# Performance work log

Hardware: AMD Instinct MI355X
Metric: run time of the kernel (lower is better)

The kernel has to match this reference:

```python
import jax, jax.numpy as jnp
import numpy as np

B, S, D, H = 2, 2048, 1024, 16  # batch, seq, rep_dim, num_heads
DH = D // H
MASK_VALUE = -1e-06  # value passed by MHAttention to masked_softmax (NOT -1e6)


def setup_inputs() -> dict:
    key = jax.random.key(0)
    ks = jax.random.split(key, 16)
    def xavier(k, shape):
        fan_in, fan_out = shape[0], shape[1]
        limit = float(np.sqrt(6.0 / (fan_in + fan_out)))
        return jax.random.uniform(k, shape, jnp.float32, -limit, limit)
    return {
        "queries": jax.random.normal(ks[0], (B, S, D), jnp.float32),
        "keys": jax.random.normal(ks[1], (B, S, D), jnp.float32),
        "values": jax.random.normal(ks[2], (B, S, D), jnp.float32),
        "thresholds": jax.random.randint(ks[3], (B,), 1, S + 1, jnp.int32),
        # Linear params stored as (in, out) so y = x @ W + b
        "Wq": xavier(ks[4], (D, D)), "bq": jnp.zeros((D,), jnp.float32),
        "Wk": xavier(ks[5], (D, D)), "bk": jnp.zeros((D,), jnp.float32),
        "Wv": xavier(ks[6], (D, D)), "bv": jnp.zeros((D,), jnp.float32),
        "W": xavier(ks[7], (DH, DH)),  # learnable bilinear attention matrix
        "Wo": xavier(ks[8], (D, D)), "bo": jnp.zeros((D,), jnp.float32),
    }


def reference(queries, keys, values, thresholds, Wq, bq, Wk, bk, Wv, bv, W, Wo, bo):
    def split_heads(x):  # (B,S,D) -> (B,H,S,DH)
        return x.reshape(B, S, H, DH).transpose(0, 2, 1, 3)

    Q = split_heads(queries @ Wq + bq)
    K = split_heads(keys @ Wk + bk)
    V = split_heads(values @ Wv + bv)

    # bilinear scores: (Q @ W) @ K^T, no 1/sqrt(d) scaling in original
    scores = jnp.einsum("bhqd,bhkd->bhqk", Q @ W, K)
    # mask key positions >= threshold[b] with MASK_VALUE before softmax
    keep = jnp.arange(S)[None, None, None, :] < thresholds[:, None, None, None]
    scores = jnp.where(keep, scores, MASK_VALUE)
    attn = jax.nn.softmax(scores, axis=-1)

    out = jnp.einsum("bhqk,bhkd->bhqd", attn, V)
    out = out.transpose(0, 2, 1, 3).reshape(B, S, D)  # merge heads
    return out @ Wo + bo
```

## Files before the change

kernel.cpp:

```cpp
#include <hip/hip_runtime.h>
#include <hip/hip_bf16.h>

#define D_MODEL 1024
#define NHEADS  16
#define DH      64
#define SEQ     2048
#define BATCH   2

#define LOG2E 1.4426950408889634f
#define MASKB2 (-1e-6f * LOG2E)
#define DEFER_THR 11.5456f
#define NEG_INF (-__builtin_inff())

typedef __attribute__((ext_vector_type(8))) short short8;
typedef __attribute__((ext_vector_type(4))) short short4v;
typedef __attribute__((ext_vector_type(4))) float f32x4;

#define AS1C(p) ((const __attribute__((address_space(1))) void*)(p))
#define AS3(p)  ((__attribute__((address_space(3))) void*)(p))

union PB { short4v s4; unsigned int u[2]; };

static __device__ __forceinline__ float fexp2(float x) {
    return __builtin_amdgcn_exp2f(x);
}

static __device__ __forceinline__ unsigned int pk2(float lo, float hi) {
    __hip_bfloat16 a = __float2bfloat16(lo), b = __float2bfloat16(hi);
    unsigned short au = *(unsigned short*)&a, bu = *(unsigned short*)&b;
    return (unsigned int)au | ((unsigned int)bu << 16);
}

__global__ __launch_bounds__(256) void fold_kernel(const float* __restrict__ Wq,
                                                   const float* __restrict__ bq,
                                                   const float* __restrict__ W,
                                                   float* __restrict__ Wq2,
                                                   float* __restrict__ bq2) {
    if (blockIdx.x < 4096) {
        int idx = blockIdx.x * 256 + threadIdx.x;
        int row = idx >> 10;
        int col = idx & 1023;
        int h = col >> 6, j = col & 63;
        const float* wqr = Wq + (size_t)row * D_MODEL + h * DH;
        float s = 0.f;
#pragma unroll
        for (int d = 0; d < DH; ++d) s += wqr[d] * W[d * DH + j];
        Wq2[idx] = s * LOG2E;
    } else {
        int col = (blockIdx.x - 4096) * 256 + threadIdx.x;
        int h = col >> 6, j = col & 63;
        float s = 0.f;
#pragma unroll
        for (int d = 0; d < DH; ++d) s += bq[h * DH + d] * W[d * DH + j];
        bq2[col] = s * LOG2E;
    }
}

__global__ __launch_bounds__(256) void convert3_kernel(const float* __restrict__ q,
                                                       const float* __restrict__ k,
                                                       const float* __restrict__ v,
                                                       __hip_bfloat16* __restrict__ oq,
                                                       __hip_bfloat16* __restrict__ ok,
                                                       __hip_bfloat16* __restrict__ ov) {
    int z = blockIdx.x >> 11;
    int i = (blockIdx.x & 2047) * 256 + threadIdx.x;
    const float* in = (z == 0) ? q : (z == 1) ? k : v;
    __hip_bfloat16* out = (z == 0) ? oq : (z == 1) ? ok : ov;
    float4 a = *(const float4*)(in + (size_t)i * 8);
    float4 b = *(const float4*)(in + (size_t)i * 8 + 4);
    __hip_bfloat16 o[8];
    o[0] = __float2bfloat16(a.x); o[1] = __float2bfloat16(a.y);
    o[2] = __float2bfloat16(a.z); o[3] = __float2bfloat16(a.w);
    o[4] = __float2bfloat16(b.x); o[5] = __float2bfloat16(b.y);
    o[6] = __float2bfloat16(b.z); o[7] = __float2bfloat16(b.w);
    *(short8*)(out + (size_t)i * 8) = *(short8*)o;
}

__global__ __launch_bounds__(256) void transpose4_kernel(const float* __restrict__ W0,
                                                         const float* __restrict__ W1,
                                                         const float* __restrict__ W2,
                                                         const float* __restrict__ W3,
                                                         __hip_bfloat16* __restrict__ T0,
                                                         __hip_bfloat16* __restrict__ T1,
                                                         __hip_bfloat16* __restrict__ T2,
                                                         __hip_bfloat16* __restrict__ T3) {
    __shared__ float sT[32][33];
    int z = blockIdx.z;
    const float* Win = (z == 0) ? W0 : (z == 1) ? W1 : (z == 2) ? W2 : W3;
    __hip_bfloat16* Wt = (z == 0) ? T0 : (z == 1) ? T1 : (z == 2) ? T2 : T3;
    int n0 = blockIdx.x * 32, k0 = blockIdx.y * 32;
    int tx = threadIdx.x & 31, ty = threadIdx.x >> 5;
#pragma unroll
    for (int i = 0; i < 4; ++i)
        sT[ty + i * 8][tx] = Win[(size_t)(k0 + ty + i * 8) * D_MODEL + n0 + tx];
    __syncthreads();
#pragma unroll
    for (int i = 0; i < 4; ++i)
        Wt[(size_t)(n0 + ty + i * 8) * D_MODEL + k0 + tx] = __float2bfloat16(sT[tx][ty + i * 8]);
}

#define GEMM_CORE(A_, BT_)                                                                  \
    __shared__ __hip_bfloat16 sA[2][128 * 32];                                              \
    __shared__ __hip_bfloat16 sB[2][128 * 32];                                              \
    const int t = threadIdx.x;                                                              \
    const int lane = t & 63, w = t >> 6;                                                    \
    const int g = lane >> 4, li = lane & 15;                                                \
    const int r0 = blockIdx.y * 128, c0 = blockIdx.x * 128;                                 \
    const int wr = (w >> 1) * 64, wc = (w & 1) * 64;                                        \
    f32x4 acc[4][4] = {};                                                                   \
    auto stage = [&](int bb, int k0) {                                                      \
        _Pragma("unroll")                                                                   \
        for (int i = 0; i < 2; ++i) {                                                       \
            int o = (i * 4 + w) * 1024 + lane * 16;                                         \
            int row = o >> 6, ce = (o & 63) >> 1;                                           \
            __builtin_amdgcn_global_load_lds(AS1C(A_ + (size_t)(r0 + row) * 1024 + k0 + ce),\
                                             AS3((char*)sA[bb] + (i * 4 + w) * 1024), 16, 0, 0); \
            __builtin_amdgcn_global_load_lds(AS1C(BT_ + (size_t)(c0 + row) * 1024 + k0 + ce),\
                                             AS3((char*)sB[bb] + (i * 4 + w) * 1024), 16, 0, 0); \
        }                                                                                   \
    };                                                                                      \
    stage(0, 0);                                                                            \
    asm volatile("s_waitcnt vmcnt(0)" ::: "memory");                                        \
    __syncthreads();                                                                        \
    int cur = 0;                                                                            \
    for (int k0 = 0; k0 < 1024; k0 += 32) {                                                 \
        if (k0 + 32 < 1024) stage(cur ^ 1, k0 + 32);                                        \
        short8 af[4], bf[4];                                                                \
        _Pragma("unroll")                                                                   \
        for (int m = 0; m < 4; ++m)                                                         \
            af[m] = *(const short8*)(sA[cur] + (wr + m * 16 + li) * 32 + g * 8);            \
        _Pragma("unroll")                                                                   \
        for (int n = 0; n < 4; ++n)                                                         \
            bf[n] = *(const short8*)(sB[cur] + (wc + n * 16 + li) * 32 + g * 8);            \
        _Pragma("unroll")                                                                   \
        for (int m = 0; m < 4; ++m)                                                         \
            _Pragma("unroll")                                                               \
            for (int n = 0; n < 4; ++n)                                                     \
                acc[m][n] = __builtin_amdgcn_mfma_f32_16x16x32_bf16(af[m], bf[n], acc[m][n], 0, 0, 0); \
        asm volatile("s_waitcnt vmcnt(0)" ::: "memory");                                    \
        __syncthreads();                                                                    \
        cur ^= 1;                                                                           \
    }

__global__ __launch_bounds__(256) void gemm_qkv_kernel(
    const __hip_bfloat16* __restrict__ Xq, const __hip_bfloat16* __restrict__ Xk,
    const __hip_bfloat16* __restrict__ Xv,
    const __hip_bfloat16* __restrict__ WqT, const __hip_bfloat16* __restrict__ WkT,
    const __hip_bfloat16* __restrict__ WvT,
    const float* __restrict__ bq2, const float* __restrict__ bk, const float* __restrict__ bv,
    __hip_bfloat16* __restrict__ Qp, __hip_bfloat16* __restrict__ Kp,
    __hip_bfloat16* __restrict__ Vt) {
    const int z = blockIdx.z;
    const __hip_bfloat16* A  = (z == 0) ? Xq  : (z == 1) ? Xk  : Xv;
    const __hip_bfloat16* BT = (z == 0) ? WqT : (z == 1) ? WkT : WvT;
    const float* bias        = (z == 0) ? bq2 : (z == 1) ? bk  : bv;
    __hip_bfloat16* C        = (z == 0) ? Qp  : (z == 1) ? Kp  : Vt;

    GEMM_CORE(A, BT)

#pragma unroll
    for (int m = 0; m < 4; ++m) {
#pragma unroll
        for (int n = 0; n < 4; ++n) {
            int col = c0 + wc + n * 16 + li;
            float bs = bias[col];
            int row0 = r0 + wr + m * 16 + g * 4;
            int h = col >> 6, d = col & 63;
            if (z == 2) {
                int b = row0 >> 11, s0 = row0 & 2047;
                __hip_bfloat16 o4[4];
#pragma unroll
                for (int r = 0; r < 4; ++r) o4[r] = __float2bfloat16(acc[m][n][r] + bs);
                *(short4*)(C + (((size_t)(b * NHEADS + h)) * DH + d) * SEQ + s0) = *(short4*)o4;
            } else {
#pragma unroll
                for (int r = 0; r < 4; ++r) {
                    int row = row0 + r;
                    int b = row >> 11, s = row & 2047;
                    C[(((size_t)(b * NHEADS + h)) * SEQ + s) * DH + d] =
                        __float2bfloat16(acc[m][n][r] + bs);
                }
            }
        }
    }
}

__global__ __launch_bounds__(256) void gemm_out_kernel(
    const __hip_bfloat16* __restrict__ A, const __hip_bfloat16* __restrict__ BT,
    const float* __restrict__ bias, float* __restrict__ C) {
    GEMM_CORE(A, BT)
#pragma unroll
    for (int m = 0; m < 4; ++m) {
#pragma unroll
        for (int n = 0; n < 4; ++n) {
            int col = c0 + wc + n * 16 + li;
            float bs = bias[col];
            int row0 = r0 + wr + m * 16 + g * 4;
#pragma unroll
            for (int r = 0; r < 4; ++r)
                C[(size_t)(row0 + r) * D_MODEL + col] = acc[m][n][r] + bs;
        }
    }
}

__global__ __launch_bounds__(256) void vsum_kernel(const __hip_bfloat16* __restrict__ Vt,
                                                   const int* __restrict__ thresholds,
                                                   float* __restrict__ Vsum) {
    int bh = blockIdx.x, b = bh >> 4;
    int thresh = thresholds[b];
    int loop_end = min(SEQ, ((thresh + 63) >> 6) << 6);
    int t = threadIdx.x;
    int dh = t >> 2, sub = t & 3;
    const __hip_bfloat16* row = Vt + ((size_t)bh * DH + dh) * SEQ;
    float s = 0.f;
    for (int s0 = loop_end + sub * 8; s0 < SEQ; s0 += 32) {
        short8 v = *(const short8*)(row + s0);
#pragma unroll
        for (int j = 0; j < 8; ++j) {
            unsigned short us = (unsigned short)v[j];
            s += __bfloat162float(*(__hip_bfloat16*)&us);
        }
    }
    s += __shfl_xor(s, 1);
    s += __shfl_xor(s, 2);
    if (sub == 0) Vsum[bh * DH + dh] = s;
}

__global__ __launch_bounds__(256) void attn_mfma_kernel(
    const __hip_bfloat16* __restrict__ Qp,
    const __hip_bfloat16* __restrict__ Kp,
    const __hip_bfloat16* __restrict__ Vt,
    const int* __restrict__ thresholds,
    const float* __restrict__ Vsum,
    __hip_bfloat16* __restrict__ AO) {
    __shared__ char lds[32768];
    char* sK  = lds;
    char* sVT = lds + 16384;

    const int t = threadIdx.x, lane = t & 63, w = t >> 6;
    const int g = lane >> 4, li = lane & 15;
    const int bh = blockIdx.x, b = bh >> 4, h = bh & 15;
    const int q0 = blockIdx.y * 64;
    const int thresh = thresholds[b];
    const int loop_end = min(SEQ, ((thresh + 63) >> 6) << 6);
    const __hip_bfloat16* Qb = Qp + (size_t)bh * SEQ * DH;
    const __hip_bfloat16* Kb = Kp + (size_t)bh * SEQ * DH;
    const __hip_bfloat16* Vb = Vt + (size_t)bh * DH * SEQ;

    short8 qf[2];
#pragma unroll
    for (int kb = 0; kb < 2; ++kb)
        qf[kb] = *(const short8*)(Qb + (size_t)(q0 + w * 16 + li) * DH + kb * 32 + g * 8);

    f32x4 Oacc[4] = {};
    float mrun = NEG_INF, lrun = 0.f;

    auto stageK = [&](int bb, int kv) {
#pragma unroll
        for (int i = 0; i < 2; ++i) {
            int o = i * 4096 + w * 1024 + lane * 16;
            int key = o >> 7, slot = (o & 127) >> 4;
            __builtin_amdgcn_global_load_lds(
                AS1C(Kb + (size_t)(kv + key) * DH + ((slot ^ (key & 7)) << 3)),
                AS3(sK + bb * 8192 + i * 4096 + w * 1024), 16, 0, 0);
        }
    };
    auto stageV = [&](int bb, int kv) {
#pragma unroll
        for (int i = 0; i < 2; ++i) {
            int o = i * 4096 + w * 1024 + lane * 16;
            int dh = o >> 7, slot = (o & 127) >> 4;
            __builtin_amdgcn_global_load_lds(
                AS1C(Vb + (size_t)dh * SEQ + kv + ((slot ^ (dh & 7)) << 3)),
                AS3(sVT + bb * 8192 + i * 4096 + w * 1024), 16, 0, 0);
        }
    };

    stageK(0, 0); stageV(0, 0);
    asm volatile("s_waitcnt vmcnt(0)" ::: "memory");
    __syncthreads();

    int cur = 0;
    for (int kv0 = 0; kv0 < loop_end; kv0 += 64) {
        int nxt = kv0 + 64;
        if (nxt < loop_end) { stageK(cur ^ 1, nxt); stageV(cur ^ 1, nxt); }

        f32x4 S[4] = {};
        __builtin_amdgcn_s_setprio(1);
#pragma unroll
        for (int kb = 0; kb < 2; ++kb) {
            short8 kf[4];
#pragma unroll
            for (int n = 0; n < 4; ++n) {
                int key = 16 * n + li;
                kf[n] = *(const short8*)(sK + cur * 8192 + key * 128 +
                                         (((4 * kb + g) ^ (key & 7)) << 4));
            }
#pragma unroll
            for (int n = 0; n < 4; ++n)
                S[n] = __builtin_amdgcn_mfma_f32_16x16x32_bf16(kf[n], qf[kb], S[n], 0, 0, 0);
        }
        __builtin_amdgcn_s_setprio(0);

        if (kv0 + 64 > thresh) {
            int tr = thresh - kv0 - 4 * g;
#pragma unroll
            for (int n = 0; n < 4; ++n)
#pragma unroll
                for (int rr = 0; rr < 4; ++rr)
                    if (16 * n + rr >= tr) S[n][rr] = MASKB2;
        }

        float mx = S[0][0];
#pragma unroll
        for (int n = 0; n < 4; ++n)
#pragma unroll
            for (int rr = 0; rr < 4; ++rr) mx = fmaxf(mx, S[n][rr]);
        mx = fmaxf(mx, __shfl_xor(mx, 16));
        mx = fmaxf(mx, __shfl_xor(mx, 32));
        float pmax = mx;

        if (__any(pmax > mrun + DEFER_THR)) {
            float mn = fmaxf(mrun, pmax);
            float alpha = fexp2(mrun - mn);
            lrun *= alpha;
#pragma unroll
            for (int n = 0; n < 4; ++n)
#pragma unroll
                for (int rr = 0; rr < 4; ++rr) Oacc[n][rr] *= alpha;
            mrun = mn;
        }

        short4v pb[4];
        float rs = 0.f;
#pragma unroll
        for (int n = 0; n < 4; ++n) {
#pragma unroll
            for (int rr = 0; rr < 4; ++rr) {
                float p = fexp2(S[n][rr] - mrun);
                S[n][rr] = p;
                rs += p;
            }
            PB u;
            u.u[0] = pk2(S[n][0], S[n][1]);
            u.u[1] = pk2(S[n][2], S[n][3]);
            pb[n] = u.s4;
        }
        rs += __shfl_xor(rs, 16);
        rs += __shfl_xor(rs, 32);
        lrun += rs;

        __builtin_amdgcn_s_setprio(1);
#pragma unroll
        for (int ks = 0; ks < 4; ++ks) {
            int slot = 2 * ks + (g >> 1);
            int sub8 = 8 * (g & 1);
#pragma unroll
            for (int n = 0; n < 4; ++n) {
                int dh = 16 * n + li;
                short4v va = *(const short4v*)(sVT + cur * 8192 + dh * 128 +
                                               ((slot ^ (dh & 7)) << 4) + sub8);
                Oacc[n] = __builtin_amdgcn_mfma_f32_16x16x16bf16_1k(va, pb[ks], Oacc[n], 0, 0, 0);
            }
        }
        __builtin_amdgcn_s_setprio(0);

        asm volatile("s_waitcnt vmcnt(0)" ::: "memory");
        __syncthreads();
        cur ^= 1;
    }

    int nmask = SEQ - loop_end;
    if (nmask > 0) {
        const float* vs = Vsum + bh * DH;
        f32x4 vsf[4];
#pragma unroll
        for (int n = 0; n < 4; ++n) vsf[n] = *(const f32x4*)(vs + 16 * n + 4 * g);
        float pu = fexp2(MASKB2 - mrun);
        lrun += (float)nmask * pu;
#pragma unroll
        for (int n = 0; n < 4; ++n)
#pragma unroll
            for (int rr = 0; rr < 4; ++rr) Oacc[n][rr] += pu * vsf[n][rr];
    }

    float linv = 1.0f / lrun;
    int q = q0 + w * 16 + li;
#pragma unroll
    for (int n = 0; n < 4; ++n) {
        __hip_bfloat16 o4[4];
#pragma unroll
        for (int rr = 0; rr < 4; ++rr) o4[rr] = __float2bfloat16(Oacc[n][rr] * linv);
        *(short4*)(AO + (size_t)(b * SEQ + q) * D_MODEL + h * DH + 16 * n + 4 * g) =
            *(short4*)o4;
    }
}

extern "C" void kernel_launch(void* const* d_in, const int* in_sizes, int n_in,
                              void* d_out, int out_size, void* d_ws, size_t ws_size,
                              hipStream_t stream) {
    const float* queries    = (const float*)d_in[0];
    const float* keys       = (const float*)d_in[1];
    const float* values     = (const float*)d_in[2];
    const int*   thresholds = (const int*)d_in[3];
    const float* Wq = (const float*)d_in[4];
    const float* bq = (const float*)d_in[5];
    const float* Wk = (const float*)d_in[6];
    const float* bk = (const float*)d_in[7];
    const float* Wv = (const float*)d_in[8];
    const float* bv = (const float*)d_in[9];
    const float* W  = (const float*)d_in[10];
    const float* Wo = (const float*)d_in[11];
    const float* bo = (const float*)d_in[12];
    float* out = (float*)d_out;

    char* wsb = (char*)d_ws;
    float* bq2  = (float*)wsb;
    float* Vsum = (float*)(wsb + 4096);
    float* Wq2  = (float*)(wsb + 16384);
    __hip_bfloat16* XqB = (__hip_bfloat16*)(wsb + 16384 + (4 << 20));
    __hip_bfloat16* XkB = XqB + (1 << 22);
    __hip_bfloat16* XvB = XkB + (1 << 22);
    __hip_bfloat16* WqT = XvB + (1 << 22);
    __hip_bfloat16* WkT = WqT + (1 << 20);
    __hip_bfloat16* WvT = WkT + (1 << 20);
    __hip_bfloat16* WoT = WvT + (1 << 20);
    __hip_bfloat16* QpB = WoT + (1 << 20);
    __hip_bfloat16* KpB = QpB + (1 << 22);
    __hip_bfloat16* VtB = KpB + (1 << 22);
    __hip_bfloat16* AOB = XqB;

    fold_kernel<<<4100, 256, 0, stream>>>(Wq, bq, W, Wq2, bq2);
    convert3_kernel<<<6144, 256, 0, stream>>>(queries, keys, values, XqB, XkB, XvB);
    transpose4_kernel<<<dim3(32, 32, 4), 256, 0, stream>>>(Wq2, Wk, Wv, Wo,
                                                           WqT, WkT, WvT, WoT);

    gemm_qkv_kernel<<<dim3(8, 32, 3), 256, 0, stream>>>(XqB, XkB, XvB, WqT, WkT, WvT,
                                                        bq2, bk, bv, QpB, KpB, VtB);
    vsum_kernel<<<32, 256, 0, stream>>>(VtB, thresholds, Vsum);

    attn_mfma_kernel<<<dim3(32, 32), 256, 0, stream>>>(QpB, KpB, VtB, thresholds, Vsum, AOB);

    gemm_out_kernel<<<dim3(8, 32), 256, 0, stream>>>(AOB, WoT, bo, out);
}
```

Measured before the change: 174.0 us.

## Fuse Wq fold with transpose, merge weight transposes and input conversion

```diff
diff --git a/kernel.cpp b/kernel.cpp
--- a/kernel.cpp
+++ b/kernel.cpp
@@ -31,72 +31,113 @@
     return (unsigned int)au | ((unsigned int)bu << 16);
 }
 
-__global__ __launch_bounds__(256) void fold_kernel(const float* __restrict__ Wq,
-                                                   const float* __restrict__ bq,
-                                                   const float* __restrict__ W,
-                                                   float* __restrict__ Wq2,
-                                                   float* __restrict__ bq2) {
-    if (blockIdx.x < 4096) {
-        int idx = blockIdx.x * 256 + threadIdx.x;
-        int row = idx >> 10;
-        int col = idx & 1023;
-        int h = col >> 6, j = col & 63;
-        const float* wqr = Wq + (size_t)row * D_MODEL + h * DH;
-        float s = 0.f;
-#pragma unroll
-        for (int d = 0; d < DH; ++d) s += wqr[d] * W[d * DH + j];
-        Wq2[idx] = s * LOG2E;
+__global__ __launch_bounds__(256) void fold_q_kernel(const float* __restrict__ Wq,
+                                                     const float* __restrict__ bq,
+                                                     const float* __restrict__ W,
+                                                     __hip_bfloat16* __restrict__ WqT,
+                                                     float* __restrict__ bq2) {
+    const int t = threadIdx.x;
+    const int c0 = blockIdx.x * 32;
+    const int h = c0 >> 6, j0 = c0 & 63;
+
+    if (blockIdx.y == 32) {
+        if (t < 32) {
+            int col = c0 + t, j = col & 63;
+            float s = 0.f;
+#pragma unroll
+            for (int d = 0; d < DH; ++d) s += bq[h * DH + d] * W[d * DH + j];
+            bq2[col] = s * LOG2E;
+        }
+        return;
+    }
+
+    const int r0 = blockIdx.y * 32;
+    __shared__ float sWq[32][68];
+    __shared__ float sW[64][36];
+    __shared__ float sOut[32][33];
+
+    {
+        int lr = t >> 3, lc8 = (t & 7) * 8;
+        const float* src = Wq + (size_t)(r0 + lr) * D_MODEL + h * DH + lc8;
+        *(float4*)&sWq[lr][lc8]     = *(const float4*)(src);
+        *(float4*)&sWq[lr][lc8 + 4] = *(const float4*)(src + 4);
+        int d = t >> 2, c8 = (t & 3) * 8;
+        const float* wsrc = W + (size_t)d * DH + j0 + c8;
+        *(float4*)&sW[d][c8]     = *(const float4*)(wsrc);
+        *(float4*)&sW[d][c8 + 4] = *(const float4*)(wsrc + 4);
+    }
+    __syncthreads();
+
+    {
+        int col_loc = t & 31, rq = t >> 5;
+        float acc0 = 0.f, acc1 = 0.f, acc2 = 0.f, acc3 = 0.f;
+#pragma unroll
+        for (int d = 0; d < 64; ++d) {
+            float wv = sW[d][col_loc];
+            acc0 += sWq[rq * 4 + 0][d] * wv;
+            acc1 += sWq[rq * 4 + 1][d] * wv;
+            acc2 += sWq[rq * 4 + 2][d] * wv;
+            acc3 += sWq[rq * 4 + 3][d] * wv;
+        }
+        sOut[col_loc][rq * 4 + 0] = acc0 * LOG2E;
+        sOut[col_loc][rq * 4 + 1] = acc1 * LOG2E;
+        sOut[col_loc][rq * 4 + 2] = acc2 * LOG2E;
+        sOut[col_loc][rq * 4 + 3] = acc3 * LOG2E;
+    }
+    __syncthreads();
+
+    {
+        int orow = t >> 3, oc4 = (t & 7) * 4;
+        __hip_bfloat16 o4[4];
+#pragma unroll
+        for (int i = 0; i < 4; ++i) o4[i] = __float2bfloat16(sOut[orow][oc4 + i]);
+        *(short4*)(WqT + (size_t)(c0 + orow) * D_MODEL + r0 + oc4) = *(short4*)o4;
+    }
+}
+
+__global__ __launch_bounds__(256) void prep_kernel(const float* __restrict__ Wk,
+                                                   const float* __restrict__ Wv,
+                                                   const float* __restrict__ Wo,
+                                                   __hip_bfloat16* __restrict__ WkT,
+                                                   __hip_bfloat16* __restrict__ WvT,
+                                                   __hip_bfloat16* __restrict__ WoT,
+                                                   const float* __restrict__ q,
+                                                   const float* __restrict__ k,
+                                                   const float* __restrict__ v,
+                                                   __hip_bfloat16* __restrict__ oq,
+                                                   __hip_bfloat16* __restrict__ ok,
+                                                   __hip_bfloat16* __restrict__ ov) {
+    __shared__ float sT[32][33];
+    int blk = blockIdx.x;
+    if (blk < 3072) {
+        int z = blk >> 10, r = blk & 1023;
+        const float* Win = (z == 0) ? Wk : (z == 1) ? Wv : Wo;
+        __hip_bfloat16* Wt = (z == 0) ? WkT : (z == 1) ? WvT : WoT;
+        int n0 = (r & 31) * 32, k0 = (r >> 5) * 32;
+        int tx = threadIdx.x & 31, ty = threadIdx.x >> 5;
+#pragma unroll
+        for (int i = 0; i < 4; ++i)
+            sT[ty + i * 8][tx] = Win[(size_t)(k0 + ty + i * 8) * D_MODEL + n0 + tx];
+        __syncthreads();
+#pragma unroll
+        for (int i = 0; i < 4; ++i)
+            Wt[(size_t)(n0 + ty + i * 8) * D_MODEL + k0 + tx] =
+                __float2bfloat16(sT[tx][ty + i * 8]);
     } else {
-        int col = (blockIdx.x - 4096) * 256 + threadIdx.x;
-        int h = col >> 6, j = col & 63;
-        float s = 0.f;
-#pragma unroll
-        for (int d = 0; d < DH; ++d) s += bq[h * DH + d] * W[d * DH + j];
-        bq2[col] = s * LOG2E;
-    }
-}
-
-__global__ __launch_bounds__(256) void convert3_kernel(const float* __restrict__ q,
-                                                       const float* __restrict__ k,
-                                                       const float* __restrict__ v,
-                                                       __hip_bfloat16* __restrict__ oq,
-                                                       __hip_bfloat16* __restrict__ ok,
-                                                       __hip_bfloat16* __restrict__ ov) {
-    int z = blockIdx.x >> 11;
-    int i = (blockIdx.x & 2047) * 256 + threadIdx.x;
-    const float* in = (z == 0) ? q : (z == 1) ? k : v;
-    __hip_bfloat16* out = (z == 0) ? oq : (z == 1) ? ok : ov;
-    float4 a = *(const float4*)(in + (size_t)i * 8);
-    float4 b = *(const float4*)(in + (size_t)i * 8 + 4);
-    __hip_bfloat16 o[8];
-    o[0] = __float2bfloat16(a.x); o[1] = __float2bfloat16(a.y);
-    o[2] = __float2bfloat16(a.z); o[3] = __float2bfloat16(a.w);
-    o[4] = __float2bfloat16(b.x); o[5] = __float2bfloat16(b.y);
-    o[6] = __float2bfloat16(b.z); o[7] = __float2bfloat16(b.w);
-    *(short8*)(out + (size_t)i * 8) = *(short8*)o;
-}
-
-__global__ __launch_bounds__(256) void transpose4_kernel(const float* __restrict__ W0,
-                                                         const float* __restrict__ W1,
-                                                         const float* __restrict__ W2,
-                                                         const float* __restrict__ W3,
-                                                         __hip_bfloat16* __restrict__ T0,
-                                                         __hip_bfloat16* __restrict__ T1,
-                                                         __hip_bfloat16* __restrict__ T2,
-                                                         __hip_bfloat16* __restrict__ T3) {
-    __shared__ float sT[32][33];
-    int z = blockIdx.z;
-    const float* Win = (z == 0) ? W0 : (z == 1) ? W1 : (z == 2) ? W2 : W3;
-    __hip_bfloat16* Wt = (z == 0) ? T0 : (z == 1) ? T1 : (z == 2) ? T2 : T3;
-    int n0 = blockIdx.x * 32, k0 = blockIdx.y * 32;
-    int tx = threadIdx.x & 31, ty = threadIdx.x >> 5;
-#pragma unroll
-    for (int i = 0; i < 4; ++i)
-        sT[ty + i * 8][tx] = Win[(size_t)(k0 + ty + i * 8) * D_MODEL + n0 + tx];
-    __syncthreads();
-#pragma unroll
-    for (int i = 0; i < 4; ++i)
-        Wt[(size_t)(n0 + ty + i * 8) * D_MODEL + k0 + tx] = __float2bfloat16(sT[tx][ty + i * 8]);
+        int idx = blk - 3072;
+        int z = idx >> 11;
+        int i = (idx & 2047) * 256 + threadIdx.x;
+        const float* in = (z == 0) ? q : (z == 1) ? k : v;
+        __hip_bfloat16* out = (z == 0) ? oq : (z == 1) ? ok : ov;
+        float4 a = *(const float4*)(in + (size_t)i * 8);
+        float4 b = *(const float4*)(in + (size_t)i * 8 + 4);
+        __hip_bfloat16 o[8];
+        o[0] = __float2bfloat16(a.x); o[1] = __float2bfloat16(a.y);
+        o[2] = __float2bfloat16(a.z); o[3] = __float2bfloat16(a.w);
+        o[4] = __float2bfloat16(b.x); o[5] = __float2bfloat16(b.y);
+        o[6] = __float2bfloat16(b.z); o[7] = __float2bfloat16(b.w);
+        *(short8*)(out + (size_t)i * 8) = *(short8*)o;
+    }
 }
 
 #define GEMM_CORE(A_, BT_)                                                                  \
@@ -239,8 +280,10 @@
 
     const int t = threadIdx.x, lane = t & 63, w = t >> 6;
     const int g = lane >> 4, li = lane & 15;
-    const int bh = blockIdx.x, b = bh >> 4, h = bh & 15;
-    const int q0 = blockIdx.y * 64;
+    const int bh_i = blockIdx.y;
+    const int bh = ((bh_i & 1) << 4) | (bh_i >> 1);
+    const int b = bh >> 4, h = bh & 15;
+    const int q0 = blockIdx.x * 64;
     const int thresh = thresholds[b];
     const int loop_end = min(SEQ, ((thresh + 63) >> 6) << 6);
     const __hip_bfloat16* Qb = Qp + (size_t)bh * SEQ * DH;
@@ -417,8 +460,7 @@
     char* wsb = (char*)d_ws;
     float* bq2  = (float*)wsb;
     float* Vsum = (float*)(wsb + 4096);
-    float* Wq2  = (float*)(wsb + 16384);
-    __hip_bfloat16* XqB = (__hip_bfloat16*)(wsb + 16384 + (4 << 20));
+    __hip_bfloat16* XqB = (__hip_bfloat16*)(wsb + 16384);
     __hip_bfloat16* XkB = XqB + (1 << 22);
     __hip_bfloat16* XvB = XkB + (1 << 22);
     __hip_bfloat16* WqT = XvB + (1 << 22);
@@ -430,10 +472,9 @@
     __hip_bfloat16* VtB = KpB + (1 << 22);
     __hip_bfloat16* AOB = XqB;
 
-    fold_kernel<<<4100, 256, 0, stream>>>(Wq, bq, W, Wq2, bq2);
-    convert3_kernel<<<6144, 256, 0, stream>>>(queries, keys, values, XqB, XkB, XvB);
-    transpose4_kernel<<<dim3(32, 32, 4), 256, 0, stream>>>(Wq2, Wk, Wv, Wo,
-                                                           WqT, WkT, WvT, WoT);
+    fold_q_kernel<<<dim3(32, 33), 256, 0, stream>>>(Wq, bq, W, WqT, bq2);
+    prep_kernel<<<9216, 256, 0, stream>>>(Wk, Wv, Wo, WkT, WvT, WoT,
+                                          queries, keys, values, XqB, XkB, XvB);
 
     gemm_qkv_kernel<<<dim3(8, 32, 3), 256, 0, stream>>>(XqB, XkB, XvB, WqT, WkT, WvT,
                                                         bq2, bk, bv, QpB, KpB, VtB);
```

After: 161.3 us. -7.3%, faster.
